# Performance work log

Hardware: AMD Instinct MI355X
Metric: run time of the kernel (lower is better)

## Reference

```python
import jax, jax.numpy as jnp
import numpy as np

N = 50000      # total nodes in batched graph
E = 800000     # total edges
G = 256        # number of graphs in batch
IN_DIM = 32
HID = 108      # hidden_dim == out_dim
N_CLASSES = 10
L = 4          # number of GraphSage layers
EPS = 1e-12


def setup_inputs() -> dict:
    key = jax.random.key(0)
    ks = jax.random.split(key, 20)
    s = 0.05
    inp = {
        'nodes_feat': jax.random.normal(ks[0], (N, IN_DIM), jnp.float32),
        'edges_feat': jax.random.normal(ks[1], (E, 1), jnp.float32),
        'nodes_num_norm_sqrt': jax.random.uniform(ks[2], (N, 1), jnp.float32),
        'edges_num_norm_sqrt': jax.random.uniform(ks[3], (E, 1), jnp.float32),
        'src': jax.random.randint(ks[4], (E,), 0, N, jnp.int32),
        'dst': jax.random.randint(ks[5], (E,), 0, N, jnp.int32),
        'graph_ids': jnp.sort(jax.random.randint(ks[6], (N,), 0, G, jnp.int32)),
        # parameters
        'W_emb': jax.random.normal(ks[7], (IN_DIM, HID), jnp.float32) * s,
        'b_emb': jnp.zeros((HID,), jnp.float32),
        'W_pool': jax.random.normal(ks[8], (L, HID, HID), jnp.float32) * s,
        'b_pool': jnp.zeros((L, HID), jnp.float32),
        'W_app': jax.random.normal(ks[9], (L, 2 * HID, HID), jnp.float32) * s,
        'b_app': jnp.zeros((L, HID), jnp.float32),
        'W_mlp1': jax.random.normal(ks[10], (HID, HID // 2), jnp.float32) * s,
        'b_mlp1': jnp.zeros((HID // 2,), jnp.float32),
        'W_mlp2': jax.random.normal(ks[11], (HID // 2, HID // 4), jnp.float32) * s,
        'b_mlp2': jnp.zeros((HID // 4,), jnp.float32),
        'W_mlp3': jax.random.normal(ks[12], (HID // 4, N_CLASSES), jnp.float32) * s,
        'b_mlp3': jnp.zeros((N_CLASSES,), jnp.float32),
    }
    return inp


def _l2norm(x):
    # F.normalize(x, p=2, dim=1)
    n = jnp.sqrt(jnp.sum(x * x, axis=1, keepdims=True))
    return x / jnp.maximum(n, EPS)


def reference(nodes_feat, edges_feat, nodes_num_norm_sqrt, edges_num_norm_sqrt,
              src, dst, graph_ids,
              W_emb, b_emb, W_pool, b_pool, W_app, b_app,
              W_mlp1, b_mlp1, W_mlp2, b_mlp2, W_mlp3, b_mlp3):
    # input embedding (dropout p=0 -> identity)
    h = nodes_feat @ W_emb + b_emb  # [N, HID]

    # in-degree per node (constant across layers)
    deg = jax.ops.segment_sum(jnp.ones((E,), h.dtype), dst, num_segments=N)
    inv_deg = (1.0 / jnp.maximum(deg, 1.0))[:, None]  # zero in-degree -> agg 0

    for l in range(L):
        h_in = h
        # meanpool aggregator: per-source linear+relu, mean over in-neighbors
        h_pool = jax.nn.relu(h @ W_pool[l] + b_pool[l])  # [N, HID]
        agg = jax.ops.segment_sum(h_pool[src], dst, num_segments=N) * inv_deg
        # NodeApply: concat(self, agg) -> linear -> L2 normalize -> relu
        bundle = jnp.concatenate([h, agg], axis=1) @ W_app[l] + b_app[l]
        h = jax.nn.relu(_l2norm(bundle))
        h = h_in + h  # residual (in_dim == out_dim for all layers)

    # dgl.mean_nodes readout over ragged graphs
    hg_sum = jax.ops.segment_sum(h, graph_ids, num_segments=G)  # [G, HID]
    cnt = jax.ops.segment_sum(jnp.ones((N,), h.dtype), graph_ids, num_segments=G)
    hg = hg_sum / jnp.maximum(cnt, 1.0)[:, None]

    # MLPReadout: 108 -> 54 -> 27 -> 10
    y = jax.nn.relu(hg @ W_mlp1 + b_mlp1)
    y = jax.nn.relu(y @ W_mlp2 + b_mlp2)
    logits = y @ W_mlp3 + b_mlp3  # [G, N_CLASSES]
    return logits
```

## Files before the change

kernel.cpp:

```cpp
#include <hip/hip_runtime.h>

#define NN 50000
#define EE 800000
#define GG 256
#define IND 32
#define HID 108
#define NL 4
#define MB 782
#define MB2 1563
#define RS 8
#define SBN 196
#define SCAP 5120
#define PCAP 6144
#define PAD 16
#define BCH 4096
#define STL 136

typedef __attribute__((ext_vector_type(8))) _Float16 f16x8;
typedef __attribute__((ext_vector_type(4))) float floatx4;
typedef __attribute__((ext_vector_type(4))) unsigned int uintx4;

__global__ void k_zero(int* p, int n) {
    int i = blockIdx.x * 256 + threadIdx.x;
    if (i < n) p[i] = 0;
}

__global__ __launch_bounds__(256)
void k_bin(const int* __restrict__ src, const int* __restrict__ dst,
           int* __restrict__ gfill, unsigned int* __restrict__ ebuf) {
    __shared__ unsigned int stage[BCH];
    __shared__ int scnt[SBN], soff[SBN], gres[SBN];
    int tid = threadIdx.x;
    int e0 = blockIdx.x * BCH;
    for (int i = tid; i < SBN; i += 256) scnt[i] = 0;
    __syncthreads();
    unsigned int pay[16]; int psb[16];
    #pragma unroll
    for (int j = 0; j < 16; j++) {
        int e = e0 + j * 256 + tid;
        if (e < EE) {
            int d = dst[e]; int s = src[e];
            int sb = d >> 8;
            psb[j] = sb;
            pay[j] = ((unsigned)sb << 24) | ((unsigned)s << 8) | (unsigned)(d & 255);
            atomicAdd(&scnt[sb], 1);
        } else psb[j] = -1;
    }
    __syncthreads();
    if (tid == 0) {
        int run = 0;
        for (int s = 0; s < SBN; s++) { soff[s] = run; run += scnt[s]; }
    }
    __syncthreads();
    if (tid < SBN) gres[tid] = atomicAdd(&gfill[tid * PAD], scnt[tid]);
    __syncthreads();
    if (tid < SBN) scnt[tid] = 0;
    __syncthreads();
    #pragma unroll
    for (int j = 0; j < 16; j++) {
        if (psb[j] >= 0) {
            int p = soff[psb[j]] + atomicAdd(&scnt[psb[j]], 1);
            stage[p] = pay[j];
        }
    }
    __syncthreads();
    int nv = soff[SBN - 1] + scnt[SBN - 1];
    for (int i = tid; i < nv; i += 256) {
        unsigned int v = stage[i];
        int sb = v >> 24;
        int idx = gres[sb] + (i - soff[sb]);
        if (idx < SCAP) ebuf[(size_t)sb * SCAP + idx] = v & 0xFFFFFFu;
    }
}

__global__ __launch_bounds__(256)
void k_place2(const unsigned int* __restrict__ ebuf, const int* __restrict__ gfill,
              int* __restrict__ rp, unsigned short* __restrict__ cs) {
    __shared__ int outb[PCAP];
    __shared__ int cnt[256];
    __shared__ int off[256];
    __shared__ int fl[SBN];
    __shared__ int sbase;
    __shared__ int wsum[4], wexc[4];
    int sb = blockIdx.x, tid = threadIdx.x;
    if (tid < SBN) fl[tid] = gfill[tid * PAD];
    cnt[tid] = 0;
    __syncthreads();
    if (tid == 0) {
        int run = 0;
        for (int s = 0; s < sb; s++) run += fl[s];
        sbase = run;
    }
    __syncthreads();
    int nE = fl[sb]; if (nE > SCAP) nE = SCAP;
    int base = sbase;
    const unsigned int* eb = ebuf + (size_t)sb * SCAP;
    for (int i = tid; i < nE; i += 256) atomicAdd(&cnt[eb[i] & 255], 1);
    __syncthreads();
    int v = cnt[tid];
    int lane = tid & 63, wv = tid >> 6;
    int x = v;
    #pragma unroll
    for (int o = 1; o < 64; o <<= 1) {
        int y = __shfl_up(x, o, 64);
        if (lane >= o) x += y;
    }
    if (lane == 63) wsum[wv] = x;
    __syncthreads();
    if (tid == 0) { int run = 0; for (int w = 0; w < 4; w++) { wexc[w] = run; run += wsum[w]; } }
    __syncthreads();
    int myoff = wexc[wv] + x - v;
    off[tid] = myoff;
    int n = (sb << 8) + tid;
    if (n <= NN) rp[n] = base + myoff;
    cnt[tid] = 0;
    __syncthreads();
    if (nE <= PCAP) {
        for (int i = tid; i < nE; i += 256) {
            unsigned int e = eb[i];
            int loc = e & 255;
            int p = atomicAdd(&cnt[loc], 1);
            outb[off[loc] + p] = (int)(e >> 8);
        }
        __syncthreads();
        for (int i = tid; i < nE; i += 256) cs[base + i] = (unsigned short)outb[i];
    } else {
        for (int i = tid; i < nE; i += 256) {
            unsigned int e = eb[i];
            int loc = e & 255;
            int p = atomicAdd(&cnt[loc], 1);
            cs[base + off[loc] + p] = (unsigned short)(e >> 8);
        }
    }
}

__global__ void k_pack(const float* __restrict__ W_pool, const float* __restrict__ b_pool,
                       const float* __restrict__ W_app, const float* __restrict__ b_app,
                       const float* __restrict__ W_emb, const float* __restrict__ b_emb,
                       _Float16* Bt1, _Float16* BtA, float* bbP, float* bbA,
                       _Float16* BtE, float* bbE) {
    int r = blockIdx.x * 256 + threadIdx.x;
    if (r < NL * 128 * 128) {
        int l = r / (128 * 128); int t = r % (128 * 128); int n = t / 128, k = t % 128;
        float v = (n < HID && k < HID) ? W_pool[((size_t)l * HID + k) * HID + n] : 0.f;
        Bt1[r] = (_Float16)v; return;
    } r -= NL * 128 * 128;
    if (r < NL * 108 * 256) {
        int l = r / (108 * 256); int t = r % (108 * 256); int n = t / 256, k = t % 256;
        float v = 0.f;
        if (k < HID)                        v = W_app[((size_t)l * 216 + k) * HID + n];
        else if (k >= 128 && k < 128 + HID) v = W_app[((size_t)l * 216 + 108 + (k - 128)) * HID + n];
        BtA[r] = (_Float16)v; return;
    } r -= NL * 108 * 256;
    if (r < NL * 128) { int l = r / 128, n = r % 128; bbP[r] = (n < HID) ? b_pool[l * HID + n] : 0.f; return; } r -= NL * 128;
    if (r < NL * 128) { int l = r / 128, n = r % 128; bbA[r] = (n < HID) ? b_app[l * HID + n] : 0.f; return; } r -= NL * 128;
    if (r < 128 * 32) {
        int n = r / 32, k = r % 32;
        BtE[r] = (n < HID) ? (_Float16)W_emb[k * HID + n] : (_Float16)0.f; return;
    } r -= 128 * 32;
    if (r < 128) { bbE[r] = (r < HID) ? b_emb[r] : 0.f; }
}

__global__ __launch_bounds__(256)
void k_embed2(const float* __restrict__ feat, const _Float16* __restrict__ BtE,
              const float* __restrict__ bias,
              const _Float16* __restrict__ Bt1n, const float* __restrict__ bbPn,
              _Float16* __restrict__ h16, _Float16* __restrict__ hp16) {
    __shared__ _Float16 Bl[128 * 32];
    __shared__ _Float16 stg[64 * STL];
    int tid = threadIdx.x;
    for (int i = tid; i < 128 * 32 / 8; i += 256)
        ((uintx4*)Bl)[i] = ((const uintx4*)BtE)[i];
    __syncthreads();
    int lane = tid & 63, wid = tid >> 6, lm = lane & 15, lq = lane >> 4;
    int m0 = blockIdx.x * 64;
    floatx4 acc[4][2];
    #pragma unroll
    for (int mi = 0; mi < 4; mi++)
        #pragma unroll
        for (int ni = 0; ni < 2; ni++) { floatx4 z = {0.f,0.f,0.f,0.f}; acc[mi][ni] = z; }
    f16x8 a[4], b[2];
    #pragma unroll
    for (int mi = 0; mi < 4; mi++) {
        int row = m0 + mi * 16 + lm;
        f16x8 av;
        if (row < NN) {
            const float4 v0 = *(const float4*)(feat + (size_t)row * 32 + lq * 8);
            const float4 v1 = *(const float4*)(feat + (size_t)row * 32 + lq * 8 + 4);
            av[0] = (_Float16)v0.x; av[1] = (_Float16)v0.y;
            av[2] = (_Float16)v0.z; av[3] = (_Float16)v0.w;
            av[4] = (_Float16)v1.x; av[5] = (_Float16)v1.y;
            av[6] = (_Float16)v1.z; av[7] = (_Float16)v1.w;
        } else {
            #pragma unroll
            for (int j = 0; j < 8; j++) av[j] = (_Float16)0.f;
        }
        a[mi] = av;
    }
    #pragma unroll
    for (int ni = 0; ni < 2; ni++) {
        int col = wid * 32 + ni * 16 + lm;
        b[ni] = *(const f16x8*)&Bl[col * 32 + lq * 8];
    }
    #pragma unroll
    for (int mi = 0; mi < 4; mi++)
        #pragma unroll
        for (int ni = 0; ni < 2; ni++)
            acc[mi][ni] = __builtin_amdgcn_mfma_f32_16x16x32_f16(a[mi], b[ni], acc[mi][ni], 0, 0, 0);
    #pragma unroll
    for (int mi = 0; mi < 4; mi++)
        #pragma unroll
        for (int ni = 0; ni < 2; ni++) {
            int col = wid * 32 + ni * 16 + lm;
            float bc = bias[col];
            #pragma unroll
            for (int r = 0; r < 4; r++) {
                int rl = mi * 16 + lq * 4 + r;
                int row = m0 + rl;
                float v = acc[mi][ni][r] + bc;
                stg[rl * STL + col] = (_Float16)v;
                if (row < NN) h16[(size_t)row * 128 + col] = (_Float16)v;
            }
        }
    __syncthreads();
    floatx4 pacc[4][2];
    #pragma unroll
    for (int mi = 0; mi < 4; mi++)
        #pragma unroll
        for (int ni = 0; ni < 2; ni++) { floatx4 z = {0.f,0.f,0.f,0.f}; pacc[mi][ni] = z; }
    #pragma unroll
    for (int ks = 0; ks < 4; ks++) {
        f16x8 pa[4], pb[2];
        #pragma unroll
        for (int mi = 0; mi < 4; mi++)
            pa[mi] = *(const f16x8*)&stg[(mi * 16 + lm) * STL + ks * 32 + lq * 8];
        #pragma unroll
        for (int ni = 0; ni < 2; ni++)
            pb[ni] = *(const f16x8*)(Bt1n + (size_t)(wid * 32 + ni * 16 + lm) * 128 + ks * 32 + lq * 8);
        #pragma unroll
        for (int mi = 0; mi < 4; mi++)
            #pragma unroll
            for (int ni = 0; ni < 2; ni++)
                pacc[mi][ni] = __builtin_amdgcn_mfma_f32_16x16x32_f16(pa[mi], pb[ni], pacc[mi][ni], 0, 0, 0);
    }
    #pragma unroll
    for (int mi = 0; mi < 4; mi++)
        #pragma unroll
        for (int ni = 0; ni < 2; ni++) {
            int col = wid * 32 + ni * 16 + lm;
            float bc = bbPn[col];
            #pragma unroll
            for (int r = 0; r < 4; r++) {
                int row = m0 + mi * 16 + lq * 4 + r;
                if (row < NN)
                    hp16[((size_t)wid * NN + row) * 32 + ni * 16 + lm] =
                        (_Float16)fmaxf(pacc[mi][ni][r] + bc, 0.f);
            }
        }
}

__global__ __launch_bounds__(256)
void k_agg3(const _Float16* __restrict__ hp16, const int* __restrict__ rp,
            const unsigned short* __restrict__ cs, _Float16* __restrict__ agg16) {
    int bid = blockIdx.x;
    int bkt = bid >> 2;
    int slice = bid & 3;
    int tid = threadIdx.x;
    int wv = tid >> 6, lane = tid & 63;
    int split = lane >> 5;
    int l5 = lane & 31;
    int nsub = l5 >> 2, c = l5 & 3;
    int n = bkt * 32 + wv * 8 + nsub;
    if (n < NN) {
        int s0 = rp[n], s1 = rp[n + 1];
        float acc[8];
        #pragma unroll
        for (int j = 0; j < 8; j++) acc[j] = 0.f;
        const _Float16* hb = hp16 + (size_t)slice * NN * 32 + c * 8;
        int e = s0 + split * 4;
        for (; e + 4 <= s1; e += 8) {
            int r0 = __builtin_nontemporal_load(cs + e);
            int r1 = __builtin_nontemporal_load(cs + e + 1);
            int r2 = __builtin_nontemporal_load(cs + e + 2);
            int r3 = __builtin_nontemporal_load(cs + e + 3);
            f16x8 v0 = *(const f16x8*)(hb + (size_t)r0 * 32);
            f16x8 v1 = *(const f16x8*)(hb + (size_t)r1 * 32);
            f16x8 v2 = *(const f16x8*)(hb + (size_t)r2 * 32);
            f16x8 v3 = *(const f16x8*)(hb + (size_t)r3 * 32);
            #pragma unroll
            for (int j = 0; j < 8; j++)
                acc[j] += ((float)v0[j] + (float)v1[j]) + ((float)v2[j] + (float)v3[j]);
        }
        for (int t = e; t < s1 && t < e + 4; t++) {
            int r0 = __builtin_nontemporal_load(cs + t);
            f16x8 v0 = *(const f16x8*)(hb + (size_t)r0 * 32);
            #pragma unroll
            for (int j = 0; j < 8; j++) acc[j] += (float)v0[j];
        }
        #pragma unroll
        for (int j = 0; j < 8; j++) acc[j] += __shfl_xor(acc[j], 32, 64);
        if (split == 0) {
            int dg = s1 - s0;
            float inv = 1.0f / (float)((dg > 1) ? dg : 1);
            f16x8 o;
            #pragma unroll
            for (int j = 0; j < 8; j++) o[j] = (_Float16)(acc[j] * inv);
            uintx4 ov = *(uintx4*)&o;
            __builtin_nontemporal_store(ov, (uintx4*)(agg16 + (size_t)n * 128 + slice * 32 + c * 8));
        }
    }
}

__global__ __launch_bounds__(256, 6)
void k_appmm1(const _Float16* __restrict__ Ah, const _Float16* __restrict__ Ag,
              const _Float16* __restrict__ Bt, const float* __restrict__ bias,
              const _Float16* __restrict__ Bt1n, const float* __restrict__ bbPn,
              float* __restrict__ h, _Float16* __restrict__ h16,
              _Float16* __restrict__ hp16, int do_mm1) {
    __shared__ float ssl[32 * 4];
    __shared__ float scl[32];
    __shared__ _Float16 lsbuf[2 * 32 * STL];
    _Float16* lA0 = lsbuf;
    _Float16* lA1 = lsbuf + 32 * STL;
    _Float16* stg = lsbuf;
    int tid = threadIdx.x;
    int lane = tid & 63, wid = tid >> 6, lm = lane & 15, lq = lane >> 4;
    int m0 = blockIdx.x * 32;
    f16x8 sv[4];
    #pragma unroll
    for (int i = 0; i < 4; i++) {
        int id = tid + 256 * i;
        int t = id >> 9;
        int rr = (id >> 4) & 31;
        int cb = id & 15;
        const _Float16* Asrc = t ? Ag : Ah;
        int grow = m0 + rr;
        if (grow >= NN) grow = 0;
        sv[i] = *(const f16x8*)(Asrc + (size_t)grow * 128 + cb * 8);
    }
    #pragma unroll
    for (int i = 0; i < 4; i++) {
        int id = tid + 256 * i;
        int t = id >> 9;
        int rr = (id >> 4) & 31;
        int cb = id & 15;
        *(f16x8*)&lsbuf[(size_t)t * 32 * STL + rr * STL + cb * 8] = sv[i];
    }
    __syncthreads();
    int colv[2], colc[2], cval[2];
    #pragma unroll
    for (int ni = 0; ni < 2; ni++) {
        int col = wid * 32 + ni * 16 + lm;
        colv[ni] = col;
        cval[ni] = (col < HID);
        colc[ni] = cval[ni] ? col : 0;
    }
    floatx4 acc[2][2];
    #pragma unroll
    for (int mi = 0; mi < 2; mi++)
        #pragma unroll
        for (int ni = 0; ni < 2; ni++) { floatx4 z = {0.f,0.f,0.f,0.f}; acc[mi][ni] = z; }
    #pragma unroll
    for (int ks = 0; ks < 8; ks++) {
        const _Float16* lsrc = (ks < 4) ? lA0 : lA1;
        int ko = (ks & 3) * 32 + lq * 8;
        f16x8 a[2], b[2];
        #pragma unroll
        for (int mi = 0; mi < 2; mi++)
            a[mi] = *(const f16x8*)&lsrc[(mi * 16 + lm) * STL + ko];
        #pragma unroll
        for (int ni = 0; ni < 2; ni++)
            b[ni] = *(const f16x8*)(Bt + (size_t)colc[ni] * 256 + ks * 32 + lq * 8);
        #pragma unroll
        for (int mi = 0; mi < 2; mi++)
            #pragma unroll
            for (int ni = 0; ni < 2; ni++)
                acc[mi][ni] = __builtin_amdgcn_mfma_f32_16x16x32_f16(a[mi], b[ni], acc[mi][ni], 0, 0, 0);
    }
    float hres[2][2][4];
    #pragma unroll
    for (int mi = 0; mi < 2; mi++)
        #pragma unroll
        for (int ni = 0; ni < 2; ni++)
            #pragma unroll
            for (int r = 0; r < 4; r++) {
                int rl = mi * 16 + lq * 4 + r;
                hres[mi][ni][r] = cval[ni] ? (float)lA0[rl * STL + colv[ni]] : 0.f;
            }
    float ss[2][4];
    #pragma unroll
    for (int mi = 0; mi < 2; mi++)
        #pragma unroll
        for (int r = 0; r < 4; r++) {
            float bc0 = bias[colv[0]];
            float bc1 = bias[colv[1]];
            acc[mi][0][r] += bc0;
            acc[mi][1][r] += bc1;
            float c0 = cval[0] ? acc[mi][0][r] : 0.f;
            float c1 = cval[1] ? acc[mi][1][r] : 0.f;
            ss[mi][r] = c0 * c0 + c1 * c1;
        }
    #pragma unroll
    for (int off = 1; off < 16; off <<= 1)
        #pragma unroll
        for (int mi = 0; mi < 2; mi++)
            #pragma unroll
            for (int r = 0; r < 4; r++)
                ss[mi][r] += __shfl_xor(ss[mi][r], off, 64);
    if (lm == 0) {
        #pragma unroll
        for (int mi = 0; mi < 2; mi++)
            #pragma unroll
            for (int r = 0; r < 4; r++)
                ssl[(mi * 16 + lq * 4 + r) * 4 + wid] = ss[mi][r];
    }
    __syncthreads();
    if (tid < 32) {
        float s = ssl[tid * 4] + ssl[tid * 4 + 1] + ssl[tid * 4 + 2] + ssl[tid * 4 + 3];
        scl[tid] = 1.0f / fmaxf(sqrtf(s), 1e-12f);
    }
    __syncthreads();
    #pragma unroll
    for (int mi = 0; mi < 2; mi++)
        #pragma unroll
        for (int ni = 0; ni < 2; ni++) {
            int col = colv[ni];
            #pragma unroll
            for (int r = 0; r < 4; r++) {
                int rl = mi * 16 + lq * 4 + r;
                int row = m0 + rl;
                float hn = 0.f;
                if (cval[ni] && row < NN) {
                    float v = fmaxf(acc[mi][ni][r] * scl[rl], 0.f);
                    hn = hres[mi][ni][r] + v;
                    if (!do_mm1) h[(size_t)row * HID + col] = hn;
                    h16[(size_t)row * 128 + col] = (_Float16)hn;
                }
                stg[rl * STL + col] = (_Float16)hn;
            }
        }
    if (do_mm1) {
        __syncthreads();
        floatx4 pacc[2][2];
        #pragma unroll
        for (int mi = 0; mi < 2; mi++)
            #pragma unroll
            for (int ni = 0; ni < 2; ni++) { floatx4 z = {0.f,0.f,0.f,0.f}; pacc[mi][ni] = z; }
        #pragma unroll
        for (int ks = 0; ks < 4; ks++) {
            f16x8 pa[2], pb[2];
            #pragma unroll
            for (int mi = 0; mi < 2; mi++)
                pa[mi] = *(const f16x8*)&stg[(mi * 16 + lm) * STL + ks * 32 + lq * 8];
            #pragma unroll
            for (int ni = 0; ni < 2; ni++)
                pb[ni] = *(const f16x8*)(Bt1n + (size_t)colv[ni] * 128 + ks * 32 + lq * 8);
            #pragma unroll
            for (int mi = 0; mi < 2; mi++)
                #pragma unroll
                for (int ni = 0; ni < 2; ni++)
                    pacc[mi][ni] = __builtin_amdgcn_mfma_f32_16x16x32_f16(pa[mi], pb[ni], pacc[mi][ni], 0, 0, 0);
        }
        #pragma unroll
        for (int mi = 0; mi < 2; mi++)
            #pragma unroll
            for (int ni = 0; ni < 2; ni++) {
                float bc = bbPn[colv[ni]];
                #pragma unroll
                for (int r = 0; r < 4; r++) {
                    int row = m0 + mi * 16 + lq * 4 + r;
                    if (row < NN)
                        hp16[((size_t)wid * NN + row) * 32 + ni * 16 + lm] =
                            (_Float16)fmaxf(pacc[mi][ni][r] + bc, 0.f);
                }
            }
    }
}

__global__ __launch_bounds__(128)
void k_seg(const float* __restrict__ h, const int* __restrict__ gid,
           float* __restrict__ hgp) {
    __shared__ int se[2];
    int g = blockIdx.x, sl = blockIdx.y, tid = threadIdx.x;
    if (tid < 2) {
        int key = g + tid, lo = 0, hi = NN;
        while (lo < hi) {
            int mid = (lo + hi) >> 1;
            if (gid[mid] < key) lo = mid + 1; else hi = mid;
        }
        se[tid] = lo;
    }
    __syncthreads();
    int s = se[0], e = se[1];
    int cnt = e - s;
    int chunk = (cnt + RS - 1) / RS;
    int ls = s + sl * chunk;
    int le = min(e, ls + chunk);
    if (tid < HID) {
        float acc = 0.f;
        for (int n = ls; n < le; n++) acc += h[(size_t)n * HID + tid];
        hgp[((size_t)g * RS + sl) * HID + tid] = acc;
    }
}

__global__ __launch_bounds__(128)
void k_mlp(const float* __restrict__ hgp, const int* __restrict__ gid,
           const float* __restrict__ W1, const float* __restrict__ b1,
           const float* __restrict__ W2, const float* __restrict__ b2,
           const float* __restrict__ W3, const float* __restrict__ b3,
           float* __restrict__ out) {
    __shared__ float hg[HID];
    __shared__ float y1[54];
    __shared__ float y2[27];
    __shared__ int se[2];
    int g = blockIdx.x, tid = threadIdx.x;
    if (tid < 2) {
        int key = g + tid, lo = 0, hi = NN;
        while (lo < hi) {
            int mid = (lo + hi) >> 1;
            if (gid[mid] < key) lo = mid + 1; else hi = mid;
        }
        se[tid] = lo;
    }
    __syncthreads();
    int cnt = se[1] - se[0];
    if (tid < HID) {
        float acc = 0.f;
        #pragma unroll
        for (int sl = 0; sl < RS; sl++) acc += hgp[((size_t)g * RS + sl) * HID + tid];
        hg[tid] = acc / (float)((cnt > 1) ? cnt : 1);
    }
    __syncthreads();
    if (tid < 54) {
        float a = b1[tid];
        for (int k = 0; k < HID; k++) a += hg[k] * W1[k * 54 + tid];
        y1[tid] = fmaxf(a, 0.f);
    }
    __syncthreads();
    if (tid < 27) {
        float a = b2[tid];
        for (int k = 0; k < 54; k++) a += y1[k] * W2[k * 27 + tid];
        y2[tid] = fmaxf(a, 0.f);
    }
    __syncthreads();
    if (tid < 10) {
        float a = b3[tid];
        for (int k = 0; k < 27; k++) a += y2[k] * W3[k * 10 + tid];
        out[g * 10 + tid] = a;
    }
}

extern "C" void kernel_launch(void* const* d_in, const int* in_sizes, int n_in,
                              void* d_out, int out_size, void* d_ws, size_t ws_size,
                              hipStream_t stream) {
    float* out = (float*)d_out;
    (void)in_sizes; (void)n_in; (void)ws_size; (void)out_size;

    const float* feat   = (const float*)d_in[0];
    const int*   src    = (const int*)d_in[4];
    const int*   dst    = (const int*)d_in[5];
    const int*   gid    = (const int*)d_in[6];
    const float* W_emb  = (const float*)d_in[7];
    const float* b_emb  = (const float*)d_in[8];
    const float* W_pool = (const float*)d_in[9];
    const float* b_pool = (const float*)d_in[10];
    const float* W_app  = (const float*)d_in[11];
    const float* b_app  = (const float*)d_in[12];
    const float* W1     = (const float*)d_in[13];
    const float* b1     = (const float*)d_in[14];
    const float* W2     = (const float*)d_in[15];
    const float* b2     = (const float*)d_in[16];
    const float* W3     = (const float*)d_in[17];
    const float* b3     = (const float*)d_in[18];

    char* ws = (char*)d_ws;
    size_t off = 0;
    auto take = [&](size_t bytes) { char* p = ws + off; off += (bytes + 255) & ~(size_t)255; return p; };
    float*     h     = (float*)take((size_t)NN * HID * 4);
    _Float16*  h16   = (_Float16*)take((size_t)NN * 128 * 2);
    _Float16*  hp16  = (_Float16*)take((size_t)4 * NN * 32 * 2);
    _Float16*  agg16 = (_Float16*)take((size_t)NN * 128 * 2);
    unsigned short* cs = (unsigned short*)take((size_t)EE * 2);
    unsigned int* ebuf = (unsigned int*)take((size_t)SBN * SCAP * 4);
    int*       rp    = (int*)take((size_t)(NN + 1) * 4);
    int*       gfill = (int*)take((size_t)SBN * PAD * 4);
    float*     hgp   = (float*)take((size_t)GG * RS * HID * 4);
    _Float16*  Bt1   = (_Float16*)take((size_t)NL * 128 * 128 * 2);
    _Float16*  BtA   = (_Float16*)take((size_t)NL * 108 * 256 * 2);
    float*     bbP   = (float*)take((size_t)NL * 128 * 4);
    float*     bbA   = (float*)take((size_t)NL * 128 * 4);
    _Float16*  BtE   = (_Float16*)take((size_t)128 * 32 * 2);
    float*     bbE   = (float*)take((size_t)128 * 4);

    hipLaunchKernelGGL(k_zero, dim3((SBN * PAD + 255) / 256), dim3(256), 0, stream,
                       gfill, SBN * PAD);
    hipLaunchKernelGGL(k_bin, dim3((EE + BCH - 1) / BCH), dim3(256), 0, stream,
                       src, dst, gfill, ebuf);
    hipLaunchKernelGGL(k_place2, dim3(SBN), dim3(256), 0, stream, ebuf, gfill, rp, cs);

    const int PACK_TOTAL = NL * 128 * 128 + NL * 108 * 256 + NL * 128 + NL * 128 + 128 * 32 + 128;
    hipLaunchKernelGGL(k_pack, dim3((PACK_TOTAL + 255) / 256), dim3(256), 0, stream,
                       W_pool, b_pool, W_app, b_app, W_emb, b_emb,
                       Bt1, BtA, bbP, bbA, BtE, bbE);

    hipLaunchKernelGGL(k_embed2, dim3(MB), dim3(256), 0, stream,
                       feat, BtE, bbE, Bt1, bbP, h16, hp16);

    for (int l = 0; l < NL; l++) {
        hipLaunchKernelGGL(k_agg3, dim3(4 * MB2), dim3(256), 0, stream,
                           hp16, rp, cs, agg16);
        int next = (l + 1 < NL) ? 1 : 0;
        hipLaunchKernelGGL(k_appmm1, dim3(MB2), dim3(256), 0, stream,
                           h16, agg16, BtA + (size_t)l * 108 * 256, bbA + (size_t)l * 128,
                           Bt1 + (size_t)(l + 1 < NL ? l + 1 : 0) * 128 * 128,
                           bbP + (size_t)(l + 1 < NL ? l + 1 : 0) * 128,
                           h, h16, hp16, next);
    }
    hipLaunchKernelGGL(k_seg, dim3(GG, RS), dim3(128), 0, stream, h, gid, hgp);
    hipLaunchKernelGGL(k_mlp, dim3(GG), dim3(128), 0, stream,
                       hgp, gid, W1, b1, W2, b2, W3, b3, out);
}
```

Measured before the change: 415.3 us.

## Parallelize bin prefix sums, deepen agg unroll, prefetch B fragments in appmm1

Replaces the serial single-thread prefix loops in k_bin and k_place2 with wave-shuffle scans and reductions. Adds an 8-edge-per-lane unrolled gather loop in k_agg3 to keep more loads in flight. In k_appmm1 it loads all B weight fragments and bias into registers before the A tile staging, so global weight loads overlap the LDS fill. It also lowers the occupancy hint from 6 to 4 blocks to make room for the extra registers, which may reduce latency hiding.

```diff
diff --git a/kernel.cpp b/kernel.cpp
--- a/kernel.cpp
+++ b/kernel.cpp
@@ -30,6 +30,7 @@
            int* __restrict__ gfill, unsigned int* __restrict__ ebuf) {
     __shared__ unsigned int stage[BCH];
     __shared__ int scnt[SBN], soff[SBN], gres[SBN];
+    __shared__ int wsum[4], wexc[4];
     int tid = threadIdx.x;
     int e0 = blockIdx.x * BCH;
     for (int i = tid; i < SBN; i += 256) scnt[i] = 0;
@@ -47,9 +48,20 @@
         } else psb[j] = -1;
     }
     __syncthreads();
-    if (tid == 0) {
-        int run = 0;
-        for (int s = 0; s < SBN; s++) { soff[s] = run; run += scnt[s]; }
+    {
+        int lane = tid & 63, wv = tid >> 6;
+        int v = (tid < SBN) ? scnt[tid] : 0;
+        int x = v;
+        #pragma unroll
+        for (int o = 1; o < 64; o <<= 1) {
+            int y = __shfl_up(x, o, 64);
+            if (lane >= o) x += y;
+        }
+        if (lane == 63) wsum[wv] = x;
+        __syncthreads();
+        if (tid == 0) { int run = 0; for (int w = 0; w < 4; w++) { wexc[w] = run; run += wsum[w]; } }
+        __syncthreads();
+        if (tid < SBN) soff[tid] = wexc[wv] + x - v;
     }
     __syncthreads();
     if (tid < SBN) gres[tid] = atomicAdd(&gfill[tid * PAD], scnt[tid]);
@@ -80,20 +92,22 @@
     __shared__ int cnt[256];
     __shared__ int off[256];
     __shared__ int fl[SBN];
-    __shared__ int sbase;
+    __shared__ int sred[4];
     __shared__ int wsum[4], wexc[4];
     int sb = blockIdx.x, tid = threadIdx.x;
     if (tid < SBN) fl[tid] = gfill[tid * PAD];
     cnt[tid] = 0;
     __syncthreads();
-    if (tid == 0) {
-        int run = 0;
-        for (int s = 0; s < sb; s++) run += fl[s];
-        sbase = run;
-    }
-    __syncthreads();
+    {
+        int lane = tid & 63, wv = tid >> 6;
+        int v = (tid < sb) ? fl[tid] : 0;
+        #pragma unroll
+        for (int o = 1; o < 64; o <<= 1) v += __shfl_xor(v, o, 64);
+        if (lane == 0) sred[wv] = v;
+    }
+    __syncthreads();
+    int base = sred[0] + sred[1] + sred[2] + sred[3];
     int nE = fl[sb]; if (nE > SCAP) nE = SCAP;
-    int base = sbase;
     const unsigned int* eb = ebuf + (size_t)sb * SCAP;
     for (int i = tid; i < nE; i += 256) atomicAdd(&cnt[eb[i] & 255], 1);
     __syncthreads();
@@ -278,6 +292,20 @@
         for (int j = 0; j < 8; j++) acc[j] = 0.f;
         const _Float16* hb = hp16 + (size_t)slice * NN * 32 + c * 8;
         int e = s0 + split * 4;
+        for (; e + 12 <= s1; e += 16) {
+            int ra[8];
+            #pragma unroll
+            for (int u = 0; u < 4; u++) ra[u] = __builtin_nontemporal_load(cs + e + u);
+            #pragma unroll
+            for (int u = 0; u < 4; u++) ra[4 + u] = __builtin_nontemporal_load(cs + e + 8 + u);
+            f16x8 v[8];
+            #pragma unroll
+            for (int u = 0; u < 8; u++) v[u] = *(const f16x8*)(hb + (size_t)ra[u] * 32);
+            #pragma unroll
+            for (int j = 0; j < 8; j++)
+                acc[j] += (((float)v[0][j] + (float)v[1][j]) + ((float)v[2][j] + (float)v[3][j]))
+                        + (((float)v[4][j] + (float)v[5][j]) + ((float)v[6][j] + (float)v[7][j]));
+        }
         for (; e + 4 <= s1; e += 8) {
             int r0 = __builtin_nontemporal_load(cs + e);
             int r1 = __builtin_nontemporal_load(cs + e + 1);
@@ -311,7 +339,7 @@
     }
 }
 
-__global__ __launch_bounds__(256, 6)
+__global__ __launch_bounds__(256, 4)
 void k_appmm1(const _Float16* __restrict__ Ah, const _Float16* __restrict__ Ag,
               const _Float16* __restrict__ Bt, const float* __restrict__ bias,
               const _Float16* __restrict__ Bt1n, const float* __restrict__ bbPn,
@@ -326,6 +354,22 @@
     int tid = threadIdx.x;
     int lane = tid & 63, wid = tid >> 6, lm = lane & 15, lq = lane >> 4;
     int m0 = blockIdx.x * 32;
+    int colv[2], colc[2], cval[2];
+    #pragma unroll
+    for (int ni = 0; ni < 2; ni++) {
+        int col = wid * 32 + ni * 16 + lm;
+        colv[ni] = col;
+        cval[ni] = (col < HID);
+        colc[ni] = cval[ni] ? col : 0;
+    }
+    f16x8 bf[8][2];
+    #pragma unroll
+    for (int ks = 0; ks < 8; ks++)
+        #pragma unroll
+        for (int ni = 0; ni < 2; ni++)
+            bf[ks][ni] = *(const f16x8*)(Bt + (size_t)colc[ni] * 256 + ks * 32 + lq * 8);
+    float bc0 = bias[colv[0]];
+    float bc1 = bias[colv[1]];
     f16x8 sv[4];
     #pragma unroll
     for (int i = 0; i < 4; i++) {
@@ -347,14 +391,6 @@
         *(f16x8*)&lsbuf[(size_t)t * 32 * STL + rr * STL + cb * 8] = sv[i];
     }
     __syncthreads();
-    int colv[2], colc[2], cval[2];
-    #pragma unroll
-    for (int ni = 0; ni < 2; ni++) {
-        int col = wid * 32 + ni * 16 + lm;
-        colv[ni] = col;
-        cval[ni] = (col < HID);
-        colc[ni] = cval[ni] ? col : 0;
-    }
     floatx4 acc[2][2];
     #pragma unroll
     for (int mi = 0; mi < 2; mi++)
@@ -364,18 +400,15 @@
     for (int ks = 0; ks < 8; ks++) {
         const _Float16* lsrc = (ks < 4) ? lA0 : lA1;
         int ko = (ks & 3) * 32 + lq * 8;
-        f16x8 a[2], b[2];
+        f16x8 a[2];
         #pragma unroll
         for (int mi = 0; mi < 2; mi++)
             a[mi] = *(const f16x8*)&lsrc[(mi * 16 + lm) * STL + ko];
         #pragma unroll
-        for (int ni = 0; ni < 2; ni++)
-            b[ni] = *(const f16x8*)(Bt + (size_t)colc[ni] * 256 + ks * 32 + lq * 8);
-        #pragma unroll
         for (int mi = 0; mi < 2; mi++)
             #pragma unroll
             for (int ni = 0; ni < 2; ni++)
-                acc[mi][ni] = __builtin_amdgcn_mfma_f32_16x16x32_f16(a[mi], b[ni], acc[mi][ni], 0, 0, 0);
+                acc[mi][ni] = __builtin_amdgcn_mfma_f32_16x16x32_f16(a[mi], bf[ks][ni], acc[mi][ni], 0, 0, 0);
     }
     float hres[2][2][4];
     #pragma unroll
@@ -392,8 +425,6 @@
     for (int mi = 0; mi < 2; mi++)
         #pragma unroll
         for (int r = 0; r < 4; r++) {
-            float bc0 = bias[colv[0]];
-            float bc1 = bias[colv[1]];
             acc[mi][0][r] += bc0;
             acc[mi][1][r] += bc1;
             float c0 = cval[0] ? acc[mi][0][r] : 0.f;
```

After: 431.9 us. 1.04x slower.
